# Kernel optimization log

Measured on AMD Instinct MI355X. Metric: run time of the kernel, lower is better.

The kernel has to match this reference:

```python
import jax, jax.numpy as jnp
import numpy as np

B, NLAT, NLON = 32, 721, 1440


def setup_inputs() -> dict:
    key = jax.random.key(0)
    k1, k2 = jax.random.split(key)
    lsm = jax.random.randint(k1, (B, NLAT, NLON), 0, 2).astype(jnp.int32)  # 0=ocean, 1=land
    vals = jax.random.normal(k2, (B, NLAT, NLON), dtype=jnp.float32)
    sst = jnp.where(lsm == 0, vals, jnp.nan)  # NaN over land, like real SST fields
    return {"sst": sst, "lsm": lsm}


def _circular_fill(sst, lsm):
    # Vectorized equivalent of the per-row masked circular linear interpolation.
    # On a uniform periodic lon grid, lon distances are proportional to circular
    # index distances, so interp1d over the tripled-longitude ocean points reduces
    # to: for each lon j, find previous/next ocean index (circularly) and lerp.
    L = sst.shape[-1]
    f32 = sst.dtype
    m = (lsm == 0) & ~jnp.isnan(sst)                       # ocean mask [B,H,L]
    ar = jnp.arange(L, dtype=jnp.int32)

    # previous ocean index <= j (circular wrap via last ocean point - L)
    a_prev = jnp.where(m, ar, -1)
    prev = jax.lax.cummax(a_prev, axis=2)
    last = prev[..., -1:]
    prev = jnp.where(prev < 0, last - L, prev)

    # next ocean index >= j (circular wrap via first ocean point + L)
    a_next = jnp.where(m, ar, 2 * L)
    nxt = jax.lax.cummin(a_next, axis=2, reverse=True)
    first = nxt[..., :1]
    nxt = jnp.where(nxt >= 2 * L, first + L, nxt)

    sst_prev = jnp.take_along_axis(sst, prev % L, axis=2)
    sst_next = jnp.take_along_axis(sst, nxt % L, axis=2)

    dtot = nxt - prev                                       # >= 0; 0 exactly at ocean points
    dp = ar - prev                                          # >= 0
    t = jnp.where(dtot > 0,
                  dp.astype(f32) / jnp.maximum(dtot, 1).astype(f32),
                  jnp.zeros((), f32))
    v = sst_prev * (1.0 - t) + sst_next * t                 # single-ocean-point rows -> constant
    row_valid = m.any(axis=2, keepdims=True)
    v = jnp.where(row_valid, v, jnp.nan)                    # no ocean points -> NaN row

    # Fill all latitude rows after the last valid row with that row's values
    H = sst.shape[1]
    hidx = jnp.arange(H, dtype=jnp.int32)
    lastrow = jnp.max(jnp.where(row_valid[..., 0], hidx[None, :], -1), axis=1)  # [B]
    bidx = jnp.arange(sst.shape[0])
    fill = v[bidx, jnp.clip(lastrow, 0)]                    # [B, L]
    cond = (hidx[None, :, None] > lastrow[:, None, None]) & (lastrow[:, None, None] >= 0)
    v = jnp.where(cond, fill[:, None, :], v)

    # Restore original SST wherever it was valid (ocean_mask = ~isnan(sst))
    return jnp.where(jnp.isnan(sst), v, sst)


def reference(sst, lsm):
    return _circular_fill(sst, lsm)
```

## Files before the change

kernel.cpp:

```cpp
#include <hip/hip_runtime.h>
#include <cstdint>

#define LON 1440
#define LAT 721
#define NB  32
#define NW32 45
#define NV   360
#define RPB 4
#define BS  (RPB * 64)

typedef float f32x4 __attribute__((ext_vector_type(4)));

__device__ __forceinline__ bool is_nan_f(float v) {
    return (__float_as_uint(v) & 0x7fffffffu) > 0x7f800000u;
}

__device__ __forceinline__ unsigned pack_nib(f32x4 v) {
    return (!is_nan_f(v.x) ? 1u : 0u) | (!is_nan_f(v.y) ? 2u : 0u)
         | (!is_nan_f(v.z) ? 4u : 0u) | (!is_nan_f(v.w) ? 8u : 0u);
}

__global__ __launch_bounds__(BS, 8) void fill_rows(const f32x4* __restrict__ sst4,
                                                   const float* __restrict__ sst,
                                                   f32x4*       __restrict__ out4,
                                                   unsigned char* __restrict__ rowflag) {
    __shared__ unsigned int msk[RPB][48];

    const int tid  = threadIdx.x;
    const int lane = tid & 63;
    const int wv   = tid >> 6;
    const int r    = blockIdx.x * RPB + wv;
    const size_t base4   = (size_t)r * NV;
    const size_t rowbase = (size_t)r * LON;

    f32x4 sv[6];
    unsigned nib[6];
    #pragma unroll
    for (int k = 0; k < 6; ++k) {
        const int c = 64 * k + lane;
        if (c < NV) {
            sv[k] = sst4[base4 + c];
            nib[k] = pack_nib(sv[k]);
        } else {
            sv[k] = (f32x4){0.f, 0.f, 0.f, 0.f};
            nib[k] = 0u;
        }
    }

    #pragma unroll
    for (int k = 0; k < 6; ++k) {
        unsigned part = nib[k] << (4 * (lane & 7));
        part |= __shfl_xor(part, 1);
        part |= __shfl_xor(part, 2);
        part |= __shfl_xor(part, 4);
        const int w = 8 * k + (lane >> 3);
        if ((lane & 7) == 0 && w < NW32) msk[wv][w] = part;
    }
    asm volatile("s_waitcnt lgkmcnt(0)" ::: "memory");

    int first = -1, last = -1;
    for (int w = 0; w < NW32; ++w) {
        unsigned mw = msk[wv][w];
        if (mw) { first = w * 32 + (__ffs(mw) - 1); break; }
    }
    if (first >= 0) {
        for (int w = NW32 - 1; w >= 0; --w) {
            unsigned mw = msk[wv][w];
            if (mw) { last = w * 32 + (31 - __clz(mw)); break; }
        }
    }
    if (lane == 0) rowflag[r] = (first >= 0) ? 1 : 0;

    #pragma unroll
    for (int k = 0; k < 6; ++k) {
        const int c = 64 * k + lane;
        if (c >= NV) continue;
        f32x4 rv = sv[k];
        const unsigned nb = nib[k];
        if (first >= 0 && nb != 0xFu) {
            const int w = c >> 3;
            const unsigned mw = msk[wv][w];
            float res[4] = {rv.x, rv.y, rv.z, rv.w};
            #pragma unroll
            for (int j = 0; j < 4; ++j) {
                if (!(nb & (1u << j))) {
                    const int i = 4 * c + j;
                    const int bpos = i & 31;
                    unsigned bits = mw & (0xffffffffu >> (31 - bpos));
                    int ww = w;
                    while (bits == 0u && ww > 0) bits = msk[wv][--ww];
                    int prev = bits ? (ww * 32 + (31 - __clz(bits)))
                                    : (last - LON);
                    bits = mw & (0xffffffffu << bpos);
                    ww = w;
                    while (bits == 0u && ww < NW32 - 1) bits = msk[wv][++ww];
                    int nxt = bits ? (ww * 32 + (__ffs(bits) - 1))
                                   : (first + LON);
                    float t  = (float)(i - prev)
                             * __builtin_amdgcn_rcpf((float)(nxt - prev));
                    float sp = sst[rowbase + (prev < 0    ? prev + LON : prev)];
                    float sn = sst[rowbase + (nxt  >= LON ? nxt  - LON : nxt)];
                    res[j] = fmaf(t, sn - sp, sp);
                }
            }
            rv.x = res[0]; rv.y = res[1]; rv.z = res[2]; rv.w = res[3];
        }
        __builtin_nontemporal_store(rv, (f32x4*)&out4[base4 + c]);
    }
}

__global__ __launch_bounds__(256) void fill_tail(const float* __restrict__ sst,
                                                 float*       __restrict__ out,
                                                 const unsigned char* __restrict__ rowflag) {
    const int b = blockIdx.x;
    const int tid = threadIdx.x;
    __shared__ int red[256];
    int lr = -1;
    for (int h = tid; h < LAT; h += 256)
        if (rowflag[b * LAT + h]) lr = h;
    red[tid] = lr;
    __syncthreads();
    for (int off = 128; off > 0; off >>= 1) {
        if (tid < off) red[tid] = max(red[tid], red[tid + off]);
        __syncthreads();
    }
    lr = red[0];
    if (lr < 0 || lr == LAT - 1) return;
    const size_t fb = ((size_t)b * LAT + lr) * LON;
    for (int h = lr + 1; h < LAT; ++h) {
        const size_t base = ((size_t)b * LAT + h) * LON;
        for (int i = tid; i < LON; i += 256) {
            float svv = sst[base + i];
            out[base + i] = is_nan_f(svv) ? out[fb + i] : svv;
        }
    }
}

extern "C" void kernel_launch(void* const* d_in, const int* in_sizes, int n_in,
                              void* d_out, int out_size, void* d_ws, size_t ws_size,
                              hipStream_t stream) {
    const f32x4* sst4 = (const f32x4*)d_in[0];
    f32x4* out4 = (f32x4*)d_out;
    unsigned char* rowflag = (unsigned char*)d_ws;

    fill_rows<<<(NB * LAT) / RPB, BS, 0, stream>>>(sst4, (const float*)d_in[0],
                                                   out4, rowflag);
    fill_tail<<<NB, 256, 0, stream>>>((const float*)d_in[0], (float*)d_out, rowflag);
}
```

Measured before the change: 304.6 us.

## Stage row in LDS for neighbor gathers and use 64-bit window mask search

Each row is copied into shared memory as it is loaded, so the prev/next ocean-value gathers read LDS instead of issuing scattered global loads. The per-point neighbor search now first checks a 64-bit window made of adjacent mask words and only falls back to the word-by-word loop when that window has no ocean point. Rows per block drop from 4 to 2 and the occupancy hint is removed. Shared memory per block grows to about 11.5KB, which may cap occupancy, and no barrier orders the LDS row writes before the cross-lane reads beyond the existing lgkmcnt wait.

```diff
diff --git a/kernel.cpp b/kernel.cpp
--- a/kernel.cpp
+++ b/kernel.cpp
@@ -6,7 +6,7 @@
 #define NB  32
 #define NW32 45
 #define NV   360
-#define RPB 4
+#define RPB 2
 #define BS  (RPB * 64)
 
 typedef float f32x4 __attribute__((ext_vector_type(4)));
@@ -20,18 +20,16 @@
          | (!is_nan_f(v.z) ? 4u : 0u) | (!is_nan_f(v.w) ? 8u : 0u);
 }
 
-__global__ __launch_bounds__(BS, 8) void fill_rows(const f32x4* __restrict__ sst4,
-                                                   const float* __restrict__ sst,
-                                                   f32x4*       __restrict__ out4,
-                                                   unsigned char* __restrict__ rowflag) {
+__global__ __launch_bounds__(BS) void fill_rows(const f32x4* __restrict__ sst4,
+                                                f32x4*       __restrict__ out4,
+                                                unsigned char* __restrict__ rowflag) {
+    __shared__ float        s[RPB][LON];
     __shared__ unsigned int msk[RPB][48];
 
-    const int tid  = threadIdx.x;
-    const int lane = tid & 63;
-    const int wv   = tid >> 6;
+    const int lane = threadIdx.x & 63;
+    const int wv   = threadIdx.x >> 6;
     const int r    = blockIdx.x * RPB + wv;
-    const size_t base4   = (size_t)r * NV;
-    const size_t rowbase = (size_t)r * LON;
+    const size_t base4 = (size_t)r * NV;
 
     f32x4 sv[6];
     unsigned nib[6];
@@ -40,6 +38,7 @@
         const int c = 64 * k + lane;
         if (c < NV) {
             sv[k] = sst4[base4 + c];
+            ((f32x4*)s[wv])[c] = sv[k];
             nib[k] = pack_nib(sv[k]);
         } else {
             sv[k] = (f32x4){0.f, 0.f, 0.f, 0.f};
@@ -76,30 +75,46 @@
         const int c = 64 * k + lane;
         if (c >= NV) continue;
         f32x4 rv = sv[k];
-        const unsigned nb = nib[k];
-        if (first >= 0 && nb != 0xFu) {
+        const unsigned nb_ = nib[k];
+        if (first >= 0 && nb_ != 0xFu) {
             const int w = c >> 3;
-            const unsigned mw = msk[wv][w];
+            const unsigned mw   = msk[wv][w];
+            const unsigned mwm1 = (w > 0)        ? msk[wv][w - 1] : 0u;
+            const unsigned mwp1 = (w < NW32 - 1) ? msk[wv][w + 1] : 0u;
+            const unsigned long long p64 =
+                ((unsigned long long)mw   << 32) | mwm1;
+            const unsigned long long n64 =
+                ((unsigned long long)mwp1 << 32) | mw;
             float res[4] = {rv.x, rv.y, rv.z, rv.w};
             #pragma unroll
             for (int j = 0; j < 4; ++j) {
-                if (!(nb & (1u << j))) {
+                if (!(nb_ & (1u << j))) {
                     const int i = 4 * c + j;
                     const int bpos = i & 31;
-                    unsigned bits = mw & (0xffffffffu >> (31 - bpos));
-                    int ww = w;
-                    while (bits == 0u && ww > 0) bits = msk[wv][--ww];
-                    int prev = bits ? (ww * 32 + (31 - __clz(bits)))
+                    unsigned long long pb = p64 & (~0ull >> (31 - bpos));
+                    int prev;
+                    if (pb) {
+                        prev = (w - 1) * 32 + (63 - __clzll(pb));
+                    } else {
+                        int ww = w - 1; unsigned bits = 0u;
+                        while (bits == 0u && ww > 0) bits = msk[wv][--ww];
+                        prev = bits ? ww * 32 + (31 - __clz(bits))
                                     : (last - LON);
-                    bits = mw & (0xffffffffu << bpos);
-                    ww = w;
-                    while (bits == 0u && ww < NW32 - 1) bits = msk[wv][++ww];
-                    int nxt = bits ? (ww * 32 + (__ffs(bits) - 1))
+                    }
+                    unsigned long long nbits = n64 >> bpos;
+                    int nxt;
+                    if (nbits) {
+                        nxt = i + (__ffsll((unsigned long long)nbits) - 1);
+                    } else {
+                        int ww = w + 1; unsigned bits = 0u;
+                        while (bits == 0u && ww < NW32 - 1) bits = msk[wv][++ww];
+                        nxt = bits ? ww * 32 + (__ffs(bits) - 1)
                                    : (first + LON);
+                    }
                     float t  = (float)(i - prev)
                              * __builtin_amdgcn_rcpf((float)(nxt - prev));
-                    float sp = sst[rowbase + (prev < 0    ? prev + LON : prev)];
-                    float sn = sst[rowbase + (nxt  >= LON ? nxt  - LON : nxt)];
+                    float sp = s[wv][prev < 0    ? prev + LON : prev];
+                    float sn = s[wv][nxt  >= LON ? nxt  - LON : nxt];
                     res[j] = fmaf(t, sn - sp, sp);
                 }
             }
@@ -143,7 +158,6 @@
     f32x4* out4 = (f32x4*)d_out;
     unsigned char* rowflag = (unsigned char*)d_ws;
 
-    fill_rows<<<(NB * LAT) / RPB, BS, 0, stream>>>(sst4, (const float*)d_in[0],
-                                                   out4, rowflag);
+    fill_rows<<<(NB * LAT) / RPB, BS, 0, stream>>>(sst4, out4, rowflag);
     fill_tail<<<NB, 256, 0, stream>>>((const float*)d_in[0], (float*)d_out, rowflag);
 }
```

Measured after the change: 289.6 us. 1.05x faster.
